# Performance work log

Measured on AMD Instinct MI355X. Metric: run time of the kernel, lower is better.

Reference implementation:

```python
import jax, jax.numpy as jnp
import numpy as np

EPS = 1e-5
OFFSET_SCALE = 1.0
KPTS = 9   # 3x3 deformable kernel
GROUP = 1  # in_dim // out_dim


def _bn(x, g, b, m, v):
    # eval-mode BatchNorm2d on (B,C,H,W)
    s = g / jnp.sqrt(v + EPS)
    return x * s[None, :, None, None] + (b - m * s)[None, :, None, None]


def _dcnv4_core(value, offset, mask, offset_scale):
    # value: (B,H,W,G,Cg); offset: (B,H,W,G,K,2) as (dx,dy); mask: (B,H,W,G,K)
    B, H, W, G, Cg = value.shape
    K = mask.shape[-1]
    dt = value.dtype
    ky = jnp.repeat(jnp.arange(3) - 1, 3).astype(dt)
    kx = jnp.tile(jnp.arange(3) - 1, 3).astype(dt)
    grid = jnp.stack([kx, ky], -1)                                   # (K,2)
    base = jnp.stack(jnp.meshgrid(jnp.arange(W, dtype=dt),
                                  jnp.arange(H, dtype=dt),
                                  indexing='xy'), -1)                # (H,W,2) = (x,y)
    loc = base[None, :, :, None, None, :] + (grid + offset) * offset_scale  # (B,H,W,G,K,2)
    px, py = loc[..., 0], loc[..., 1]
    x0 = jnp.floor(px); y0 = jnp.floor(py)
    fx = px - x0; fy = py - y0
    vflat = value.transpose(0, 3, 1, 2, 4).reshape(B, G, H * W, Cg)
    out = jnp.zeros((B, G, H * W, Cg), dt)
    corners = ((0.0, 0.0, (1 - fx) * (1 - fy)), (1.0, 0.0, fx * (1 - fy)),
               (0.0, 1.0, (1 - fx) * fy), (1.0, 1.0, fx * fy))
    for dx, dy, wgt in corners:
        xi = x0 + dx; yi = y0 + dy
        valid = ((xi >= 0) & (xi < W) & (yi >= 0) & (yi < H)).astype(dt)
        idx = (jnp.clip(yi, 0, W and H - 1) * W + jnp.clip(xi, 0, W - 1)).astype(jnp.int32)
        idx = idx.transpose(0, 3, 1, 2, 4).reshape(B, G, H * W * K)
        v = jnp.take_along_axis(vflat, idx[..., None], axis=2).reshape(B, G, H * W, K, Cg)
        w = (wgt * valid * mask).transpose(0, 3, 1, 2, 4).reshape(B, G, H * W, K)
        out = out + jnp.einsum('bgsk,bgskc->bgsc', w, v)
    return out.reshape(B, G, H, W, Cg).transpose(0, 2, 3, 1, 4).reshape(B, H, W, G * Cg)


def setup_inputs() -> dict:
    key = jax.random.key(0)
    B, C, H, W = 8, 128, 64, 64
    C_OUT = 128
    OM = ((GROUP * KPTS * 3 + 7) // 8) * 8  # 32, offset_mask padded width
    ks = jax.random.split(key, 16)
    f = jnp.float32
    sc = 1.0 / np.sqrt(C).astype(np.float32)
    return {
        'x': jax.random.normal(ks[0], (B, C, H, W), f),
        'bn1_g': jax.random.uniform(ks[1], (C,), f, 0.5, 1.5),
        'bn1_b': jax.random.normal(ks[2], (C,), f) * 0.1,
        'bn1_m': jax.random.normal(ks[3], (C,), f) * 0.1,
        'bn1_v': jax.random.uniform(ks[4], (C,), f, 0.5, 1.5),
        'w_pw0': jax.random.normal(ks[5], (C, C), f) * sc,
        'w_vp': jax.random.normal(ks[6], (C, C), f) * sc,
        'b_vp': jnp.zeros((C,), f),
        'w_om': jax.random.normal(ks[7], (C, OM), f) * 0.01,
        'b_om': jnp.zeros((OM,), f),
        'w_op': jax.random.normal(ks[8], (C, C), f) * sc,
        'bn2_g': jax.random.uniform(ks[9], (C,), f, 0.5, 1.5),
        'bn2_b': jax.random.normal(ks[10], (C,), f) * 0.1,
        'bn2_m': jax.random.normal(ks[11], (C,), f) * 0.1,
        'bn2_v': jax.random.uniform(ks[12], (C,), f, 0.5, 1.5),
        'w_pw1': jax.random.normal(ks[13], (C_OUT, C), f) * sc,
    }


def reference(x, bn1_g, bn1_b, bn1_m, bn1_v, w_pw0, w_vp, b_vp, w_om, b_om, w_op,
              bn2_g, bn2_b, bn2_m, bn2_v, w_pw1):
    x = _bn(x, bn1_g, bn1_b, bn1_m, bn1_v)
    x = jnp.einsum('bchw,oc->bohw', x, w_pw0)
    B, C, H, W = x.shape
    x = x.reshape(B, H * W, C)  # raw reshape (faithful to torch .reshape, NOT a permute)
    G, K = GROUP, KPTS
    Cg = C // G
    value = (x @ w_vp + b_vp).reshape(B, H, W, G, Cg)
    om = (x @ w_om + b_om)[..., :G * K * 3].reshape(B, H, W, G, K, 3)
    out = _dcnv4_core(value, om[..., :2], om[..., 2], OFFSET_SCALE)
    out = out.reshape(B, H * W, C) @ w_op
    x = out.reshape(B, C, H, W)  # raw reshape back
    x = _bn(x, bn2_g, bn2_b, bn2_m, bn2_v)
    x = jnp.einsum('bchw,oc->bohw', x, w_pw1)
    return x
```

## Files before the change

### kernel.cpp

```cpp
#include <hip/hip_runtime.h>

#define HW 4096
#define PADF 33
#define PADU 136
typedef unsigned short ushort;
typedef __attribute__((ext_vector_type(8))) short short8;
typedef __attribute__((ext_vector_type(4))) float f32x4;

__device__ __forceinline__ ushort bf_rne(float f) {
  unsigned u = __float_as_uint(f);
  unsigned r = (u + 0x7fffu + ((u >> 16) & 1u)) >> 16;
  return (ushort)r;
}
__device__ __forceinline__ void split2(float f, ushort& hi, ushort& lo) {
  ushort h = bf_rne(f);
  float hf = __uint_as_float((unsigned)h << 16);
  hi = h;
  lo = bf_rne(f - hf);
}

__global__ __launch_bounds__(256) void prep(
    const float* __restrict__ g1, const float* __restrict__ be1,
    const float* __restrict__ m1, const float* __restrict__ v1,
    const float* __restrict__ w0,
    const float* __restrict__ g2, const float* __restrict__ be2,
    const float* __restrict__ m2, const float* __restrict__ v2,
    const float* __restrict__ w1,
    const float* __restrict__ wvp, const float* __restrict__ wom,
    const float* __restrict__ wop,
    ushort* __restrict__ W0h, ushort* __restrict__ W0l, float* __restrict__ b0,
    ushort* __restrict__ W1h, ushort* __restrict__ W1l, float* __restrict__ b1,
    ushort* __restrict__ vph, ushort* __restrict__ vpl,
    ushort* __restrict__ oph, ushort* __restrict__ opl,
    ushort* __restrict__ omh, ushort* __restrict__ oml)
{
  const int t = threadIdx.x;
  const int role = blockIdx.x;
  if (role < 16) {
    __shared__ float sc[128], sh[128], part[16][17];
    const int cv = role >> 3;
    const float* g  = cv ? g2 : g1;
    const float* be = cv ? be2 : be1;
    const float* mm = cv ? m2 : m1;
    const float* vv = cv ? v2 : v1;
    if (t < 128) {
      float s = g[t] / sqrtf(vv[t] + 1e-5f);
      sc[t] = s;
      sh[t] = be[t] - mm[t] * s;
    }
    __syncthreads();
    const float* ws = cv ? w1 : w0;
    ushort* dh = cv ? W1h : W0h;
    ushort* dl = cv ? W1l : W0l;
    float* bb  = cv ? b1 : b0;
    const int o = ((role & 7) << 4) + (t >> 4);
    const int kl = t & 15;
    float accb = 0.f;
    #pragma unroll
    for (int j = 0; j < 8; ++j) {
      const int k = (kl << 3) + j;
      const float wv = ws[o * 128 + k];
      ushort hi, lo;
      split2(wv * sc[k], hi, lo);
      dh[o * 128 + k] = hi;
      dl[o * 128 + k] = lo;
      accb = fmaf(wv, sh[k], accb);
    }
    part[t >> 4][kl] = accb;
    __syncthreads();
    if (kl == 0) {
      float s = 0.f;
      #pragma unroll
      for (int j = 0; j < 16; ++j) s += part[t >> 4][j];
      bb[o] = s;
    }
  } else if (role < 32) {
    const int rr = role & 7;
    const float* srcM = (role < 24) ? wvp : wop;
    ushort* dh = (role < 24) ? vph : oph;
    ushort* dl = (role < 24) ? vpl : opl;
    const int n = (rr << 4) + (t >> 4);
    const int kl = t & 15;
    #pragma unroll
    for (int j = 0; j < 8; ++j) {
      const int k = (kl << 3) + j;
      ushort hi, lo;
      split2(srcM[k * 128 + n], hi, lo);
      dh[n * 128 + k] = hi;
      dl[n * 128 + k] = lo;
    }
  } else {
    const int n = ((role - 32) << 4) + (t >> 4);
    const int kl = t & 15;
    #pragma unroll
    for (int j = 0; j < 8; ++j) {
      const int k = (kl << 3) + j;
      ushort hi, lo;
      split2(wom[k * 32 + n], hi, lo);
      omh[n * 128 + k] = hi;
      oml[n * 128 + k] = lo;
    }
  }
}

__global__ __launch_bounds__(512, 2) void fused_x_valom(
    const float* __restrict__ x,
    const ushort* __restrict__ W0h, const ushort* __restrict__ W0l,
    const float* __restrict__ b0,
    const ushort* __restrict__ vph, const ushort* __restrict__ vpl,
    const float* __restrict__ bvp, const float* __restrict__ bom,
    float* __restrict__ value, float* __restrict__ omb)
{
  __shared__ __align__(16) char smem[102912];
  __shared__ float b0_s[128], b2_s[160];
  ushort (*Wh_s)[32] = (ushort(*)[32])(smem);
  ushort (*Wl_s)[32] = (ushort(*)[32])(smem + 8192);
  float*  Xf         = (float*)(smem + 16384);
  ushort (*Vh_s)[32] = (ushort(*)[32])(smem);
  ushort (*Vl_s)[32] = (ushort(*)[32])(smem + 10240);
  ushort (*Yh)[PADU] = (ushort(*)[PADU])(smem + 33280);
  ushort (*Yl)[PADU] = (ushort(*)[PADU])(smem + 68096);

  const int t = threadIdx.x;
  const int cb = blockIdx.x;
  const int b = blockIdx.y;
  const int hwBase = cb << 7;
  const size_t xbase = (size_t)b * (size_t)(128 * HW);
  if (t < 128) b0_s[t] = b0[t];
  if (t < 160) b2_s[t] = (t < 128) ? bvp[t] : bom[t - 128];
  const int lane = t & 63, w = t >> 6;
  const int col = lane & 15, quad = lane >> 4;
  const f32x4 z = {0.f, 0.f, 0.f, 0.f};

  f32x4 acc1[8];
  #pragma unroll
  for (int f = 0; f < 8; ++f) acc1[f] = z;

  for (int kc = 0; kc < 4; ++kc) {
    const int kB = kc << 5;
    {
      const int o = t >> 2, q8 = (t & 3) << 3;
      *(uint4*)&Wh_s[o][q8] = *(const uint4*)&W0h[o * 128 + kB + q8];
      *(uint4*)&Wl_s[o][q8] = *(const uint4*)&W0l[o * 128 + kB + q8];
    }
    #pragma unroll
    for (int p = 0; p < 2; ++p) {
      const int idx = (p << 9) + t;
      const int c = idx >> 5, j4 = (idx & 31) << 2;
      const float4 f = *(const float4*)&x[xbase + (size_t)(kB + c) * HW + hwBase + j4];
      Xf[(j4 + 0) * PADF + c] = f.x;
      Xf[(j4 + 1) * PADF + c] = f.y;
      Xf[(j4 + 2) * PADF + c] = f.z;
      Xf[(j4 + 3) * PADF + c] = f.w;
    }
    __syncthreads();
    union { ushort u[8]; short8 v; } bh, bl;
    {
      const float* xr = &Xf[((w << 4) + col) * PADF + (quad << 3)];
      #pragma unroll
      for (int j = 0; j < 8; ++j) split2(xr[j], bh.u[j], bl.u[j]);
    }
    #pragma unroll
    for (int f = 0; f < 8; ++f) {
      const int row = (f << 4) + col;
      const short8 aH = *(const short8*)&Wh_s[row][quad << 3];
      const short8 aL = *(const short8*)&Wl_s[row][quad << 3];
      acc1[f] = __builtin_amdgcn_mfma_f32_16x16x32_bf16(aH, bh.v, acc1[f], 0, 0, 0);
      acc1[f] = __builtin_amdgcn_mfma_f32_16x16x32_bf16(aH, bl.v, acc1[f], 0, 0, 0);
      acc1[f] = __builtin_amdgcn_mfma_f32_16x16x32_bf16(aL, bh.v, acc1[f], 0, 0, 0);
    }
    __syncthreads();
  }

  #pragma unroll
  for (int f = 0; f < 8; ++f)
    #pragma unroll
    for (int r = 0; r < 4; ++r) {
      const int o = (f << 4) + (quad << 2) + r;
      const int j = (w << 4) + col;
      ushort hi, lo;
      split2(acc1[f][r] + b0_s[o], hi, lo);
      Yh[o][j] = hi;
      Yl[o][j] = lo;
    }

  const int wm2 = (w & 3) << 5;
  const int wn2 = (w >> 2) * 80;
  f32x4 acc2[2][5];
  #pragma unroll
  for (int i = 0; i < 2; ++i)
    #pragma unroll
    for (int j = 0; j < 5; ++j) acc2[i][j] = z;

  for (int j2 = 0; j2 < 4; ++j2) {
    for (int i = t; i < 640; i += 512) {
      const int n = i >> 2, q8 = (i & 3) << 3;
      *(uint4*)&Vh_s[n][q8] = *(const uint4*)&vph[n * 128 + (j2 << 5) + q8];
      *(uint4*)&Vl_s[n][q8] = *(const uint4*)&vpl[n * 128 + (j2 << 5) + q8];
    }
    __syncthreads();
    short8 aH[2], aL[2];
    #pragma unroll
    for (int f2 = 0; f2 < 2; ++f2) {
      const int row = wm2 + (f2 << 4) + col;
      aH[f2] = *(const short8*)&Yh[row][(j2 << 5) + (quad << 3)];
      aL[f2] = *(const short8*)&Yl[row][(j2 << 5) + (quad << 3)];
    }
    #pragma unroll
    for (int g2 = 0; g2 < 5; ++g2) {
      const int n = wn2 + (g2 << 4) + col;
      const short8 vh = *(const short8*)&Vh_s[n][quad << 3];
      const short8 vl = *(const short8*)&Vl_s[n][quad << 3];
      #pragma unroll
      for (int f2 = 0; f2 < 2; ++f2) {
        acc2[f2][g2] = __builtin_amdgcn_mfma_f32_16x16x32_bf16(aH[f2], vh, acc2[f2][g2], 0, 0, 0);
        acc2[f2][g2] = __builtin_amdgcn_mfma_f32_16x16x32_bf16(aH[f2], vl, acc2[f2][g2], 0, 0, 0);
        acc2[f2][g2] = __builtin_amdgcn_mfma_f32_16x16x32_bf16(aL[f2], vh, acc2[f2][g2], 0, 0, 0);
      }
    }
    __syncthreads();
  }
  #pragma unroll
  for (int f2 = 0; f2 < 2; ++f2)
    #pragma unroll
    for (int r = 0; r < 4; ++r) {
      const int m = wm2 + (f2 << 4) + (quad << 2) + r;
      const size_t gRow = (size_t)b * HW + (size_t)m * 32 + cb;
      #pragma unroll
      for (int g2 = 0; g2 < 5; ++g2) {
        const int n = wn2 + (g2 << 4) + col;
        const float v = acc2[f2][g2][r] + b2_s[n];
        if (n < 128) value[gRow * 128 + n] = v;
        else         omb[gRow * 32 + (n - 128)] = v;
      }
    }
}

struct __align__(8) WgtRec {
  float w00, w10, w01, w11;
  ushort i00, i10, i01, i11;
};

__global__ __launch_bounds__(512, 2) void fused_sample_op_out(
    const float* __restrict__ value, const float* __restrict__ omb,
    const ushort* __restrict__ oph, const ushort* __restrict__ opl,
    const ushort* __restrict__ W1h, const ushort* __restrict__ W1l,
    const float* __restrict__ b1, float* __restrict__ out)
{
  __shared__ __align__(16) char smem[158720];
  __shared__ float b1_s[128];
  ushort (*Afh)[128][32]  = (ushort(*)[128][32])(smem);
  ushort (*Afl)[128][32]  = (ushort(*)[128][32])(smem + 32768);
  ushort (*Bh)[128][32]   = (ushort(*)[128][32])(smem + 65536);
  ushort (*Bl)[128][32]   = (ushort(*)[128][32])(smem + 98304);
  WgtRec (*wgt)[9]        = (WgtRec(*)[9])(smem + 131072);
  ushort (*Yh)[PADU]      = (ushort(*)[PADU])(smem);
  ushort (*Yl)[PADU]      = (ushort(*)[PADU])(smem + 34816);
  ushort (*W1h_)[128][32] = (ushort(*)[128][32])(smem + 69632);
  ushort (*W1l_)[128][32] = (ushort(*)[128][32])(smem + 102400);

  const int t = threadIdx.x;
  const int blk = blockIdx.x;
  const int b = blk & 7;
  const int cb = blk >> 3;
  if (t < 128) b1_s[t] = b1[t];
  const int lane = t & 63, w = t >> 6;
  const int col = lane & 15, quad = lane >> 4;
  const f32x4 z = {0.f, 0.f, 0.f, 0.f};

  #pragma unroll
  for (int i = 0; i < 4; ++i) {
    const int idx = (i << 9) + t;
    const int kc = idx >> 9, n = (idx >> 2) & 127, q8 = (idx & 3) << 3;
    *(uint4*)&Bh[kc][n][q8] = *(const uint4*)&oph[n * 128 + (kc << 5) + q8];
    *(uint4*)&Bl[kc][n][q8] = *(const uint4*)&opl[n * 128 + (kc << 5) + q8];
  }
  for (int p = t; p < 1152; p += 512) {
    const int m = p / 9, k = p - m * 9;
    const int s = m * 32 + cb;
    const size_t ob = ((size_t)b * HW + s) * 32 + k * 3;
    const float dx = omb[ob], dy = omb[ob + 1], mw = omb[ob + 2];
    const float px = (float)(s & 63) + (float)(k % 3 - 1) + dx;
    const float py = (float)(s >> 6) + (float)(k / 3 - 1) + dy;
    const float x0f = floorf(px), y0f = floorf(py);
    const float fx = px - x0f, fy = py - y0f;
    const int ix = (int)x0f, iy = (int)y0f;
    const float vx0 = (ix >= 0 && ix < 64) ? 1.f : 0.f;
    const float vx1 = (ix >= -1 && ix < 63) ? 1.f : 0.f;
    const float vy0 = (iy >= 0 && iy < 64) ? 1.f : 0.f;
    const float vy1 = (iy >= -1 && iy < 63) ? 1.f : 0.f;
    const int xc0 = min(max(ix, 0), 63), xc1 = min(max(ix + 1, 0), 63);
    const int yc0 = min(max(iy, 0), 63), yc1 = min(max(iy + 1, 0), 63);
    const float gx0 = (1.f - fx) * mw * vx0;
    const float gx1 = fx * mw * vx1;
    WgtRec r;
    r.w00 = gx0 * (1.f - fy) * vy0;
    r.w10 = gx1 * (1.f - fy) * vy0;
    r.w01 = gx0 * fy * vy1;
    r.w11 = gx1 * fy * vy1;
    r.i00 = (ushort)((yc0 << 6) + xc0);
    r.i10 = (ushort)((yc0 << 6) + xc1);
    r.i01 = (ushort)((yc1 << 6) + xc0);
    r.i11 = (ushort)((yc1 << 6) + xc1);
    wgt[m][k] = r;
  }
  __syncthreads();

  {
    const int xhalf = lane >> 5;
    const int c4 = (lane & 31) << 2;
    const float* vb = value + (size_t)b * (size_t)(HW * 128) + c4;
    const int kcw = (lane & 31) >> 3;
    const int cow = (lane & 7) << 2;
    #pragma unroll 2
    for (int tt = 0; tt < 16; ++tt) {
      const int m = (w << 4) + tt;
      float a0 = 0.f, a1 = 0.f, a2 = 0.f, a3 = 0.f;
      #pragma unroll
      for (int k = 0; k < 9; ++k) {
        const WgtRec r = wgt[m][k];
        const float wA = xhalf ? r.w10 : r.w00;
        const float wB = xhalf ? r.w11 : r.w01;
        const int iA = xhalf ? (int)r.i10 : (int)r.i00;
        const int iB = xhalf ? (int)r.i11 : (int)r.i01;
        const float4 v0 = *(const float4*)&vb[(size_t)iA * 128];
        const float4 v1 = *(const float4*)&vb[(size_t)iB * 128];
        a0 = fmaf(wA, v0.x, a0); a1 = fmaf(wA, v0.y, a1);
        a2 = fmaf(wA, v0.z, a2); a3 = fmaf(wA, v0.w, a3);
        a0 = fmaf(wB, v1.x, a0); a1 = fmaf(wB, v1.y, a1);
        a2 = fmaf(wB, v1.z, a2); a3 = fmaf(wB, v1.w, a3);
      }
      a0 += __shfl_xor(a0, 32); a1 += __shfl_xor(a1, 32);
      a2 += __shfl_xor(a2, 32); a3 += __shfl_xor(a3, 32);
      if (!xhalf) {
        ushort h0, l0, h1, l1, h2, l2, h3, l3;
        split2(a0, h0, l0); split2(a1, h1, l1);
        split2(a2, h2, l2); split2(a3, h3, l3);
        uint2 uh, ul;
        uh.x = (unsigned)h0 | ((unsigned)h1 << 16);
        uh.y = (unsigned)h2 | ((unsigned)h3 << 16);
        ul.x = (unsigned)l0 | ((unsigned)l1 << 16);
        ul.y = (unsigned)l2 | ((unsigned)l3 << 16);
        *(uint2*)&Afh[kcw][m][cow] = uh;
        *(uint2*)&Afl[kcw][m][cow] = ul;
      }
    }
  }
  __syncthreads();

  const int nW = t >> 2, q8W = (t & 3) << 3;
  uint4 w1rH[4], w1rL[4];
  #pragma unroll
  for (int ii = 0; ii < 4; ++ii) {
    w1rH[ii] = *(const uint4*)&W1h[nW * 128 + (ii << 5) + q8W];
    w1rL[ii] = *(const uint4*)&W1l[nW * 128 + (ii << 5) + q8W];
  }

  const int wm1 = (w & 1) << 6, wn1 = (w >> 1) << 5;
  f32x4 acc1[4][2];
  #pragma unroll
  for (int i = 0; i < 4; ++i) { acc1[i][0] = z; acc1[i][1] = z; }

  #pragma unroll 1
  for (int kc = 0; kc < 4; ++kc) {
    short8 aH[4], aL[4];
    #pragma unroll
    for (int f = 0; f < 4; ++f) {
      const int row = wm1 + (f << 4) + col;
      aH[f] = *(const short8*)&Afh[kc][row][quad << 3];
      aL[f] = *(const short8*)&Afl[kc][row][quad << 3];
    }
    #pragma unroll
    for (int g = 0; g < 2; ++g) {
      const int n = wn1 + (g << 4) + col;
      const short8 bh = *(const short8*)&Bh[kc][n][quad << 3];
      const short8 bl = *(const short8*)&Bl[kc][n][quad << 3];
      #pragma unroll
      for (int f = 0; f < 4; ++f) {
        acc1[f][g] = __builtin_amdgcn_mfma_f32_16x16x32_bf16(aH[f], bh, acc1[f][g], 0, 0, 0);
        acc1[f][g] = __builtin_amdgcn_mfma_f32_16x16x32_bf16(aH[f], bl, acc1[f][g], 0, 0, 0);
        acc1[f][g] = __builtin_amdgcn_mfma_f32_16x16x32_bf16(aL[f], bh, acc1[f][g], 0, 0, 0);
      }
    }
  }
  __syncthreads();

  #pragma unroll
  for (int ii = 0; ii < 4; ++ii) {
    *(uint4*)&W1h_[ii][nW][q8W] = w1rH[ii];
    *(uint4*)&W1l_[ii][nW][q8W] = w1rL[ii];
  }
  #pragma unroll
  for (int f = 0; f < 4; ++f)
    #pragma unroll
    for (int g = 0; g < 2; ++g) {
      const int j   = wn1 + (g << 4) + col;
      const int chb = wm1 + (f << 4) + (quad << 2);
      ushort h0, l0, h1, l1, h2, l2, h3, l3;
      split2(acc1[f][g][0], h0, l0); split2(acc1[f][g][1], h1, l1);
      split2(acc1[f][g][2], h2, l2); split2(acc1[f][g][3], h3, l3);
      uint2 uh, ul;
      uh.x = (unsigned)h0 | ((unsigned)h1 << 16);
      uh.y = (unsigned)h2 | ((unsigned)h3 << 16);
      ul.x = (unsigned)l0 | ((unsigned)l1 << 16);
      ul.y = (unsigned)l2 | ((unsigned)l3 << 16);
      *(uint2*)&Yh[j][chb] = uh;
      *(uint2*)&Yl[j][chb] = ul;
    }
  __syncthreads();

  const int wm2 = (w & 1) << 6, wn2 = (w >> 1) << 5;
  f32x4 acc2[4][2];
  #pragma unroll
  for (int i = 0; i < 4; ++i) { acc2[i][0] = z; acc2[i][1] = z; }

  #pragma unroll 1
  for (int j2 = 0; j2 < 4; ++j2) {
    short8 aH[4], aL[4];
    #pragma unroll
    for (int f2 = 0; f2 < 4; ++f2) {
      const int row = wm2 + (f2 << 4) + col;
      aH[f2] = *(const short8*)&W1h_[j2][row][quad << 3];
      aL[f2] = *(const short8*)&W1l_[j2][row][quad << 3];
    }
    #pragma unroll
    for (int g2 = 0; g2 < 2; ++g2) {
      const int j = wn2 + (g2 << 4) + col;
      const short8 bh = *(const short8*)&Yh[j][(j2 << 5) + (quad << 3)];
      const short8 bl = *(const short8*)&Yl[j][(j2 << 5) + (quad << 3)];
      #pragma unroll
      for (int f2 = 0; f2 < 4; ++f2) {
        acc2[f2][g2] = __builtin_amdgcn_mfma_f32_16x16x32_bf16(aH[f2], bh, acc2[f2][g2], 0, 0, 0);
        acc2[f2][g2] = __builtin_amdgcn_mfma_f32_16x16x32_bf16(aH[f2], bl, acc2[f2][g2], 0, 0, 0);
        acc2[f2][g2] = __builtin_amdgcn_mfma_f32_16x16x32_bf16(aL[f2], bh, acc2[f2][g2], 0, 0, 0);
      }
    }
  }
  const size_t obase = (size_t)b * (size_t)(128 * HW) + ((size_t)cb << 7);
  #pragma unroll
  for (int f2 = 0; f2 < 4; ++f2)
    #pragma unroll
    for (int r = 0; r < 4; ++r) {
      const int o = wm2 + (f2 << 4) + (quad << 2) + r;
      #pragma unroll
      for (int g2 = 0; g2 < 2; ++g2) {
        const int j = wn2 + (g2 << 4) + col;
        out[obase + (size_t)o * HW + j] = acc2[f2][g2][r] + b1_s[o];
      }
    }
}

extern "C" void kernel_launch(void* const* d_in, const int* in_sizes, int n_in,
                              void* d_out, int out_size, void* d_ws, size_t ws_size,
                              hipStream_t stream)
{
  const float* x    = (const float*)d_in[0];
  const float* g1   = (const float*)d_in[1];
  const float* be1  = (const float*)d_in[2];
  const float* m1   = (const float*)d_in[3];
  const float* v1   = (const float*)d_in[4];
  const float* wpw0 = (const float*)d_in[5];
  const float* wvp  = (const float*)d_in[6];
  const float* bvp  = (const float*)d_in[7];
  const float* womW = (const float*)d_in[8];
  const float* bom  = (const float*)d_in[9];
  const float* wop  = (const float*)d_in[10];
  const float* g2   = (const float*)d_in[11];
  const float* be2  = (const float*)d_in[12];
  const float* m2   = (const float*)d_in[13];
  const float* v2   = (const float*)d_in[14];
  const float* wpw1 = (const float*)d_in[15];

  char* ws = (char*)d_ws;
  float*  value = (float*) (ws + 0);
  float*  omb   = (float*) (ws + 16777216);
  size_t o = 20971520;
  ushort* W0h = (ushort*)(ws + o); o += 32768;
  ushort* W0l = (ushort*)(ws + o); o += 32768;
  ushort* W1h = (ushort*)(ws + o); o += 32768;
  ushort* W1l = (ushort*)(ws + o); o += 32768;
  ushort* vph = (ushort*)(ws + o); o += 40960;
  ushort* vpl = (ushort*)(ws + o); o += 40960;
  ushort* oph = (ushort*)(ws + o); o += 32768;
  ushort* opl = (ushort*)(ws + o); o += 32768;
  float*  b0  = (float*)(ws + o);  o += 512;
  float*  b1  = (float*)(ws + o);
  ushort* omh = vph + 128 * 128;
  ushort* oml = vpl + 128 * 128;

  prep<<<34, 256, 0, stream>>>(g1, be1, m1, v1, wpw0, g2, be2, m2, v2, wpw1,
                               wvp, womW, wop,
                               W0h, W0l, b0, W1h, W1l, b1,
                               vph, vpl, oph, opl, omh, oml);
  fused_x_valom<<<dim3(32, 8), 512, 0, stream>>>(x, W0h, W0l, b0, vph, vpl,
                                                 bvp, bom, value, omb);
  fused_sample_op_out<<<dim3(256), 512, 0, stream>>>(value, omb, oph, opl,
                                                     W1h, W1l, b1, (float*)d_out);
}
```

Before: 148.5 us.

## Fold weight prep kernel into consumer kernels, recomputing BN-folded split weights per block

Removes the separate prep launch that precomputed BN-folded, bf16 hi/lo split weights and biases into workspace. Each block of the two main kernels now reads the fp32 weights and BN params directly, folds the BN scale and shift, splits to hi/lo and computes the bias itself. This saves one kernel launch and the serial dependency on it. In exchange every block repeats the weight conversion, with strided uncoalesced fp32 reads (e.g. the transposed wvp/wop reads) and scalar shared-memory stores.

```diff
diff --git a/kernel.cpp b/kernel.cpp
--- a/kernel.cpp
+++ b/kernel.cpp
@@ -19,100 +19,18 @@
   lo = bf_rne(f - hf);
 }
 
-__global__ __launch_bounds__(256) void prep(
+__global__ __launch_bounds__(512, 2) void fused_x_valom(
+    const float* __restrict__ x,
     const float* __restrict__ g1, const float* __restrict__ be1,
     const float* __restrict__ m1, const float* __restrict__ v1,
     const float* __restrict__ w0,
-    const float* __restrict__ g2, const float* __restrict__ be2,
-    const float* __restrict__ m2, const float* __restrict__ v2,
-    const float* __restrict__ w1,
     const float* __restrict__ wvp, const float* __restrict__ wom,
-    const float* __restrict__ wop,
-    ushort* __restrict__ W0h, ushort* __restrict__ W0l, float* __restrict__ b0,
-    ushort* __restrict__ W1h, ushort* __restrict__ W1l, float* __restrict__ b1,
-    ushort* __restrict__ vph, ushort* __restrict__ vpl,
-    ushort* __restrict__ oph, ushort* __restrict__ opl,
-    ushort* __restrict__ omh, ushort* __restrict__ oml)
-{
-  const int t = threadIdx.x;
-  const int role = blockIdx.x;
-  if (role < 16) {
-    __shared__ float sc[128], sh[128], part[16][17];
-    const int cv = role >> 3;
-    const float* g  = cv ? g2 : g1;
-    const float* be = cv ? be2 : be1;
-    const float* mm = cv ? m2 : m1;
-    const float* vv = cv ? v2 : v1;
-    if (t < 128) {
-      float s = g[t] / sqrtf(vv[t] + 1e-5f);
-      sc[t] = s;
-      sh[t] = be[t] - mm[t] * s;
-    }
-    __syncthreads();
-    const float* ws = cv ? w1 : w0;
-    ushort* dh = cv ? W1h : W0h;
-    ushort* dl = cv ? W1l : W0l;
-    float* bb  = cv ? b1 : b0;
-    const int o = ((role & 7) << 4) + (t >> 4);
-    const int kl = t & 15;
-    float accb = 0.f;
-    #pragma unroll
-    for (int j = 0; j < 8; ++j) {
-      const int k = (kl << 3) + j;
-      const float wv = ws[o * 128 + k];
-      ushort hi, lo;
-      split2(wv * sc[k], hi, lo);
-      dh[o * 128 + k] = hi;
-      dl[o * 128 + k] = lo;
-      accb = fmaf(wv, sh[k], accb);
-    }
-    part[t >> 4][kl] = accb;
-    __syncthreads();
-    if (kl == 0) {
-      float s = 0.f;
-      #pragma unroll
-      for (int j = 0; j < 16; ++j) s += part[t >> 4][j];
-      bb[o] = s;
-    }
-  } else if (role < 32) {
-    const int rr = role & 7;
-    const float* srcM = (role < 24) ? wvp : wop;
-    ushort* dh = (role < 24) ? vph : oph;
-    ushort* dl = (role < 24) ? vpl : opl;
-    const int n = (rr << 4) + (t >> 4);
-    const int kl = t & 15;
-    #pragma unroll
-    for (int j = 0; j < 8; ++j) {
-      const int k = (kl << 3) + j;
-      ushort hi, lo;
-      split2(srcM[k * 128 + n], hi, lo);
-      dh[n * 128 + k] = hi;
-      dl[n * 128 + k] = lo;
-    }
-  } else {
-    const int n = ((role - 32) << 4) + (t >> 4);
-    const int kl = t & 15;
-    #pragma unroll
-    for (int j = 0; j < 8; ++j) {
-      const int k = (kl << 3) + j;
-      ushort hi, lo;
-      split2(wom[k * 32 + n], hi, lo);
-      omh[n * 128 + k] = hi;
-      oml[n * 128 + k] = lo;
-    }
-  }
-}
-
-__global__ __launch_bounds__(512, 2) void fused_x_valom(
-    const float* __restrict__ x,
-    const ushort* __restrict__ W0h, const ushort* __restrict__ W0l,
-    const float* __restrict__ b0,
-    const ushort* __restrict__ vph, const ushort* __restrict__ vpl,
     const float* __restrict__ bvp, const float* __restrict__ bom,
     float* __restrict__ value, float* __restrict__ omb)
 {
   __shared__ __align__(16) char smem[102912];
   __shared__ float b0_s[128], b2_s[160];
+  __shared__ float sc1[128], sh1[128], part[128][4];
   ushort (*Wh_s)[32] = (ushort(*)[32])(smem);
   ushort (*Wl_s)[32] = (ushort(*)[32])(smem + 8192);
   float*  Xf         = (float*)(smem + 16384);
@@ -126,11 +44,27 @@
   const int b = blockIdx.y;
   const int hwBase = cb << 7;
   const size_t xbase = (size_t)b * (size_t)(128 * HW);
-  if (t < 128) b0_s[t] = b0[t];
+  if (t < 128) {
+    const float s = g1[t] / sqrtf(v1[t] + 1e-5f);
+    sc1[t] = s;
+    sh1[t] = be1[t] - m1[t] * s;
+  }
   if (t < 160) b2_s[t] = (t < 128) ? bvp[t] : bom[t - 128];
   const int lane = t & 63, w = t >> 6;
   const int col = lane & 15, quad = lane >> 4;
   const f32x4 z = {0.f, 0.f, 0.f, 0.f};
+  __syncthreads();
+
+  {
+    const int o = t >> 2, kq = t & 3;
+    float s = 0.f;
+    #pragma unroll
+    for (int jj = 0; jj < 32; ++jj) {
+      const int k = (kq << 5) + jj;
+      s = fmaf(w0[o * 128 + k], sh1[k], s);
+    }
+    part[o][kq] = s;
+  }
 
   f32x4 acc1[8];
   #pragma unroll
@@ -140,8 +74,14 @@
     const int kB = kc << 5;
     {
       const int o = t >> 2, q8 = (t & 3) << 3;
-      *(uint4*)&Wh_s[o][q8] = *(const uint4*)&W0h[o * 128 + kB + q8];
-      *(uint4*)&Wl_s[o][q8] = *(const uint4*)&W0l[o * 128 + kB + q8];
+      #pragma unroll
+      for (int j = 0; j < 8; ++j) {
+        const int k = kB + q8 + j;
+        ushort hi, lo;
+        split2(w0[o * 128 + k] * sc1[k], hi, lo);
+        Wh_s[o][q8 + j] = hi;
+        Wl_s[o][q8 + j] = lo;
+      }
     }
     #pragma unroll
     for (int p = 0; p < 2; ++p) {
@@ -154,6 +94,8 @@
       Xf[(j4 + 3) * PADF + c] = f.w;
     }
     __syncthreads();
+    if (kc == 0 && t < 128)
+      b0_s[t] = part[t][0] + part[t][1] + part[t][2] + part[t][3];
     union { ushort u[8]; short8 v; } bh, bl;
     {
       const float* xr = &Xf[((w << 4) + col) * PADF + (quad << 3)];
@@ -193,10 +135,18 @@
     for (int j = 0; j < 5; ++j) acc2[i][j] = z;
 
   for (int j2 = 0; j2 < 4; ++j2) {
+    const int kB = j2 << 5;
     for (int i = t; i < 640; i += 512) {
       const int n = i >> 2, q8 = (i & 3) << 3;
-      *(uint4*)&Vh_s[n][q8] = *(const uint4*)&vph[n * 128 + (j2 << 5) + q8];
-      *(uint4*)&Vl_s[n][q8] = *(const uint4*)&vpl[n * 128 + (j2 << 5) + q8];
+      #pragma unroll
+      for (int j = 0; j < 8; ++j) {
+        const int k = kB + q8 + j;
+        const float f = (n < 128) ? wvp[k * 128 + n] : wom[k * 32 + (n - 128)];
+        ushort hi, lo;
+        split2(f, hi, lo);
+        Vh_s[n][q8 + j] = hi;
+        Vl_s[n][q8 + j] = lo;
+      }
     }
     __syncthreads();
     short8 aH[2], aL[2];
@@ -243,12 +193,14 @@
 
 __global__ __launch_bounds__(512, 2) void fused_sample_op_out(
     const float* __restrict__ value, const float* __restrict__ omb,
-    const ushort* __restrict__ oph, const ushort* __restrict__ opl,
-    const ushort* __restrict__ W1h, const ushort* __restrict__ W1l,
-    const float* __restrict__ b1, float* __restrict__ out)
+    const float* __restrict__ wop,
+    const float* __restrict__ g2, const float* __restrict__ be2,
+    const float* __restrict__ m2, const float* __restrict__ v2,
+    const float* __restrict__ w1,
+    float* __restrict__ out)
 {
   __shared__ __align__(16) char smem[158720];
-  __shared__ float b1_s[128];
+  __shared__ float b1_s[128], sc2[128], sh2[128], part2[128][4];
   ushort (*Afh)[128][32]  = (ushort(*)[128][32])(smem);
   ushort (*Afl)[128][32]  = (ushort(*)[128][32])(smem + 32768);
   ushort (*Bh)[128][32]   = (ushort(*)[128][32])(smem + 65536);
@@ -263,17 +215,39 @@
   const int blk = blockIdx.x;
   const int b = blk & 7;
   const int cb = blk >> 3;
-  if (t < 128) b1_s[t] = b1[t];
   const int lane = t & 63, w = t >> 6;
   const int col = lane & 15, quad = lane >> 4;
   const f32x4 z = {0.f, 0.f, 0.f, 0.f};
 
+  if (t < 128) {
+    const float s = g2[t] / sqrtf(v2[t] + 1e-5f);
+    sc2[t] = s;
+    sh2[t] = be2[t] - m2[t] * s;
+  }
+  __syncthreads();
+
   #pragma unroll
   for (int i = 0; i < 4; ++i) {
     const int idx = (i << 9) + t;
     const int kc = idx >> 9, n = (idx >> 2) & 127, q8 = (idx & 3) << 3;
-    *(uint4*)&Bh[kc][n][q8] = *(const uint4*)&oph[n * 128 + (kc << 5) + q8];
-    *(uint4*)&Bl[kc][n][q8] = *(const uint4*)&opl[n * 128 + (kc << 5) + q8];
+    #pragma unroll
+    for (int j = 0; j < 8; ++j) {
+      const int k = (kc << 5) + q8 + j;
+      ushort hi, lo;
+      split2(wop[k * 128 + n], hi, lo);
+      Bh[kc][n][q8 + j] = hi;
+      Bl[kc][n][q8 + j] = lo;
+    }
+  }
+  {
+    const int o = t >> 2, kq = t & 3;
+    float s = 0.f;
+    #pragma unroll
+    for (int jj = 0; jj < 32; ++jj) {
+      const int k = (kq << 5) + jj;
+      s = fmaf(w1[o * 128 + k], sh2[k], s);
+    }
+    part2[o][kq] = s;
   }
   for (int p = t; p < 1152; p += 512) {
     const int m = p / 9, k = p - m * 9;
@@ -348,12 +322,13 @@
   }
   __syncthreads();
 
+  if (t < 128) b1_s[t] = part2[t][0] + part2[t][1] + part2[t][2] + part2[t][3];
   const int nW = t >> 2, q8W = (t & 3) << 3;
-  uint4 w1rH[4], w1rL[4];
+  float4 w1r[8];
   #pragma unroll
   for (int ii = 0; ii < 4; ++ii) {
-    w1rH[ii] = *(const uint4*)&W1h[nW * 128 + (ii << 5) + q8W];
-    w1rL[ii] = *(const uint4*)&W1l[nW * 128 + (ii << 5) + q8W];
+    w1r[ii * 2 + 0] = *(const float4*)&w1[nW * 128 + (ii << 5) + q8W + 0];
+    w1r[ii * 2 + 1] = *(const float4*)&w1[nW * 128 + (ii << 5) + q8W + 4];
   }
 
   const int wm1 = (w & 1) << 6, wn1 = (w >> 1) << 5;
@@ -387,8 +362,25 @@
 
   #pragma unroll
   for (int ii = 0; ii < 4; ++ii) {
-    *(uint4*)&W1h_[ii][nW][q8W] = w1rH[ii];
-    *(uint4*)&W1l_[ii][nW][q8W] = w1rL[ii];
+    ushort hs[8], ls[8];
+    #pragma unroll
+    for (int j = 0; j < 8; ++j) {
+      const int k = (ii << 5) + q8W + j;
+      const float f = ((j < 4) ? ((const float*)&w1r[ii * 2])[j]
+                               : ((const float*)&w1r[ii * 2 + 1])[j - 4]) * sc2[k];
+      split2(f, hs[j], ls[j]);
+    }
+    uint4 uh, ul;
+    uh.x = (unsigned)hs[0] | ((unsigned)hs[1] << 16);
+    uh.y = (unsigned)hs[2] | ((unsigned)hs[3] << 16);
+    uh.z = (unsigned)hs[4] | ((unsigned)hs[5] << 16);
+    uh.w = (unsigned)hs[6] | ((unsigned)hs[7] << 16);
+    ul.x = (unsigned)ls[0] | ((unsigned)ls[1] << 16);
+    ul.y = (unsigned)ls[2] | ((unsigned)ls[3] << 16);
+    ul.z = (unsigned)ls[4] | ((unsigned)ls[5] << 16);
+    ul.w = (unsigned)ls[6] | ((unsigned)ls[7] << 16);
+    *(uint4*)&W1h_[ii][nW][q8W] = uh;
+    *(uint4*)&W1l_[ii][nW][q8W] = ul;
   }
   #pragma unroll
   for (int f = 0; f < 4; ++f)
@@ -474,26 +466,10 @@
   char* ws = (char*)d_ws;
   float*  value = (float*) (ws + 0);
   float*  omb   = (float*) (ws + 16777216);
-  size_t o = 20971520;
-  ushort* W0h = (ushort*)(ws + o); o += 32768;
-  ushort* W0l = (ushort*)(ws + o); o += 32768;
-  ushort* W1h = (ushort*)(ws + o); o += 32768;
-  ushort* W1l = (ushort*)(ws + o); o += 32768;
-  ushort* vph = (ushort*)(ws + o); o += 40960;
-  ushort* vpl = (ushort*)(ws + o); o += 40960;
-  ushort* oph = (ushort*)(ws + o); o += 32768;
-  ushort* opl = (ushort*)(ws + o); o += 32768;
-  float*  b0  = (float*)(ws + o);  o += 512;
-  float*  b1  = (float*)(ws + o);
-  ushort* omh = vph + 128 * 128;
-  ushort* oml = vpl + 128 * 128;
-
-  prep<<<34, 256, 0, stream>>>(g1, be1, m1, v1, wpw0, g2, be2, m2, v2, wpw1,
-                               wvp, womW, wop,
-                               W0h, W0l, b0, W1h, W1l, b1,
-                               vph, vpl, oph, opl, omh, oml);
-  fused_x_valom<<<dim3(32, 8), 512, 0, stream>>>(x, W0h, W0l, b0, vph, vpl,
-                                                 bvp, bom, value, omb);
-  fused_sample_op_out<<<dim3(256), 512, 0, stream>>>(value, omb, oph, opl,
-                                                     W1h, W1l, b1, (float*)d_out);
+
+  fused_x_valom<<<dim3(32, 8), 512, 0, stream>>>(x, g1, be1, m1, v1, wpw0,
+                                                 wvp, womW, bvp, bom, value, omb);
+  fused_sample_op_out<<<dim3(256), 512, 0, stream>>>(value, omb, wop,
+                                                     g2, be2, m2, v2, wpw1,
+                                                     (float*)d_out);
 }
```

Result: no change. 150.8 us (+1.5%).
